# Kernel optimization log

Hardware: AMD Instinct MI355X
Metric: run time of the kernel (lower is better)

The kernel has to match this reference:

```python
import jax, jax.numpy as jnp
import numpy as np

TOPK = 2  # config.topk_exp


def setup_inputs() -> dict:
    key = jax.random.key(0)
    ks = jax.random.split(key, 4)
    B, S, D, F, E = 4, 1024, 768, 3072, 8
    scale_in = 1.0 / np.sqrt(D)
    scale_hid = 1.0 / np.sqrt(F)
    return {
        "x": jax.random.normal(ks[0], (B, S, D), dtype=jnp.float32),
        "router_w": jax.random.normal(ks[1], (E, D), dtype=jnp.float32) * scale_in,
        "w_fc": jax.random.normal(ks[2], (E, D, F), dtype=jnp.float32) * scale_in,
        "b_fc": jnp.zeros((E, F), dtype=jnp.float32),
        "w_proj": jax.random.normal(ks[3], (E, F, D), dtype=jnp.float32) * scale_hid,
        "b_proj": jnp.zeros((E, D), dtype=jnp.float32),
    }


def _moe_forward(x, router_w, w_fc, b_fc, w_proj, b_proj):
    B, S, D = x.shape
    E = router_w.shape[0]
    xt = x.reshape(-1, D)  # [T, D] tokens
    # per-token router: Linear(D, E, bias=False)
    gate_logits = xt @ router_w.T  # [T, E]
    # topk_exp > 1: raw logits -> topk -> softmax over the k selected logits
    weights, selected = jax.lax.top_k(gate_logits, TOPK)  # [T, k]
    weights = jax.nn.softmax(weights.astype(jnp.float32), axis=1).astype(x.dtype)
    # combine weights per expert: w[t, e] = sum_k weights[t,k] * (selected[t,k]==e)
    onehot = jax.nn.one_hot(selected, E, dtype=x.dtype)  # [T, k, E]
    comb = jnp.einsum('tk,tke->te', weights, onehot)  # [T, E]
    # expert MLP (GPT-2 style: fc -> gelu -> proj), evaluated densely then combined
    h = jax.nn.gelu(jnp.einsum('td,edf->etf', xt, w_fc) + b_fc[:, None, :], approximate=False)
    y = jnp.einsum('etf,efd->etd', h, w_proj) + b_proj[:, None, :]  # [E, T, D]
    out = jnp.einsum('te,etd->td', comb, y)  # weighted scatter-combine
    return out.reshape(B, S, D)


def reference(x, router_w, w_fc, b_fc, w_proj, b_proj):
    return _moe_forward(x, router_w, w_fc, b_fc, w_proj, b_proj)
```

## Files before the change

### kernel.cpp

```cpp
#include <hip/hip_runtime.h>
#include <hip/hip_bf16.h>

#define TT 4096
#define DD 768
#define FF 3072
#define EE 8
#define NSLOT 8192
#define NSLOT_PAD 8320

#define WVM0  0x0F70

typedef __attribute__((ext_vector_type(8))) short bf16x8;
typedef __attribute__((ext_vector_type(4))) float f32x4;
typedef const __attribute__((address_space(1))) void* gas1_t;
typedef __attribute__((address_space(3))) void* las3_t;

__global__ __launch_bounds__(256) void router2_kernel(const float* __restrict__ x,
    const float* __restrict__ rw, int* __restrict__ tokE, float* __restrict__ tokW,
    int* __restrict__ blkCnt) {
  __shared__ float rws[EE * 832];
  __shared__ int cnt_s[EE];
  int tid = threadIdx.x;
  if (tid < EE) cnt_s[tid] = 0;
#pragma unroll
  for (int k = 0; k < 6; ++k) {
    int c = tid + k * 256;
    int e = c / 192, rem = c % 192;
    int s = rem / 12, i = rem % 12;
    float4 v = *(const float4*)&rw[e * DD + s * 48 + i * 4];
    *(float4*)&rws[e * 832 + s * 52 + i * 4] = v;
  }
  __syncthreads();
  int lane = tid & 63;
  int sl = lane & 15;
  int t = blockIdx.x * 16 + (tid >> 6) * 4 + (lane >> 4);
  const float4* xp = (const float4*)(x + (size_t)t * DD + sl * 48);
  float acc[EE];
#pragma unroll
  for (int e = 0; e < EE; ++e) acc[e] = 0.f;
#pragma unroll
  for (int i = 0; i < 12; ++i) {
    float4 xv = xp[i];
#pragma unroll
    for (int e = 0; e < EE; ++e) {
      float4 rv = *(const float4*)&rws[e * 832 + sl * 52 + i * 4];
      acc[e] = fmaf(xv.x, rv.x, fmaf(xv.y, rv.y, fmaf(xv.z, rv.z, fmaf(xv.w, rv.w, acc[e]))));
    }
  }
#pragma unroll
  for (int off = 8; off > 0; off >>= 1) {
#pragma unroll
    for (int e = 0; e < EE; ++e) acc[e] += __shfl_xor(acc[e], off);
  }
  if (sl == 0) {
    float v0 = -1e30f; int e0 = 0;
#pragma unroll
    for (int e = 0; e < EE; ++e) { if (acc[e] > v0) { v0 = acc[e]; e0 = e; } }
    float v1 = -1e30f; int e1 = 0;
#pragma unroll
    for (int e = 0; e < EE; ++e) { if (e != e0 && acc[e] > v1) { v1 = acc[e]; e1 = e; } }
    float w1 = 1.f / (1.f + __expf(v0 - v1));
    float w0 = 1.f - w1;
    tokE[2 * t] = e0; tokE[2 * t + 1] = e1;
    tokW[2 * t] = w0; tokW[2 * t + 1] = w1;
    atomicAdd(&cnt_s[e0], 1);
    atomicAdd(&cnt_s[e1], 1);
  }
  __syncthreads();
  if (tid < EE) blkCnt[blockIdx.x * EE + tid] = cnt_s[tid];
}

__global__ __launch_bounds__(256) void offsets2_kernel(const int* __restrict__ blkCnt,
    int* __restrict__ offs, int* __restrict__ blkBase,
    int* __restrict__ tile1, int* __restrict__ tile2, int* __restrict__ meta) {
  __shared__ int wsum[4][EE];
  int tid = threadIdx.x;
  int lane = tid & 63, w = tid >> 6;
  int c[EE], s[EE];
#pragma unroll
  for (int e = 0; e < EE; ++e) { c[e] = blkCnt[tid * EE + e]; s[e] = c[e]; }
#pragma unroll
  for (int off = 1; off < 64; off <<= 1) {
#pragma unroll
    for (int e = 0; e < EE; ++e) {
      int v = __shfl_up(s[e], off);
      if (lane >= off) s[e] += v;
    }
  }
  if (lane == 63) {
#pragma unroll
    for (int e = 0; e < EE; ++e) wsum[w][e] = s[e];
  }
  __syncthreads();
#pragma unroll
  for (int e = 0; e < EE; ++e) {
    int pre = 0;
    for (int w2 = 0; w2 < w; ++w2) pre += wsum[w2][e];
    s[e] += pre;
  }
  int tot[EE];
#pragma unroll
  for (int e = 0; e < EE; ++e) tot[e] = wsum[0][e] + wsum[1][e] + wsum[2][e] + wsum[3][e];
  int offl[EE + 1];
  offl[0] = 0;
#pragma unroll
  for (int e = 0; e < EE; ++e) offl[e + 1] = offl[e] + tot[e];
#pragma unroll
  for (int e = 0; e < EE; ++e) blkBase[tid * EE + e] = offl[e] + s[e] - c[e];
  if (tid == 0) {
    for (int e = 0; e <= EE; ++e) offs[e] = offl[e];
    int n1 = 0, n2 = 0;
    for (int e = 0; e < EE; ++e) { n1 += (tot[e] + 127) / 128; n2 += (tot[e] + 63) / 64; }
    meta[0] = n1; meta[1] = n2;
  }
  if (tid < EE) {
    int p1 = 0, p2 = 0;
    for (int e = 0; e < tid; ++e) { p1 += (tot[e] + 127) / 128; p2 += (tot[e] + 63) / 64; }
    for (int m = 0; m < tot[tid]; m += 128) tile1[p1++] = (tid << 20) | m;
    for (int m = 0; m < tot[tid]; m += 64)  tile2[p2++] = (tid << 20) | m;
  }
}

__global__ __launch_bounds__(256) void scatter_gather2_kernel(const float* __restrict__ x,
    const int* __restrict__ tokE, const float* __restrict__ tokW,
    const int* __restrict__ blkBase, int* __restrict__ slotIdx, float* __restrict__ slotW,
    int* __restrict__ slotTok, __hip_bfloat16* __restrict__ Xg) {
  __shared__ int base_s[EE], lcur[EE];
  __shared__ int sl_s[16][2];
  int tid = threadIdx.x;
  int b = blockIdx.x;
  if (tid < EE) { base_s[tid] = blkBase[b * EE + tid]; lcur[tid] = 0; }
  __syncthreads();
  if (tid < 16) {
    int t = b * 16 + tid;
    int e0 = tokE[2 * t], e1 = tokE[2 * t + 1];
    int s0 = base_s[e0] + atomicAdd(&lcur[e0], 1);
    int s1 = base_s[e1] + atomicAdd(&lcur[e1], 1);
    slotIdx[2 * t] = s0; slotIdx[2 * t + 1] = s1;
    slotW[s0] = tokW[2 * t]; slotW[s1] = tokW[2 * t + 1];
    slotTok[s0] = t; slotTok[s1] = t;
    sl_s[tid][0] = s0; sl_s[tid][1] = s1;
  }
  __syncthreads();
  int k = tid >> 4, p = tid & 15;
  int t = b * 16 + k;
  int s0 = sl_s[k][0], s1 = sl_s[k][1];
  const float4* src = (const float4*)(x + (size_t)t * DD);
  ushort4* d0 = (ushort4*)(Xg + (size_t)s0 * DD);
  ushort4* d1 = (ushort4*)(Xg + (size_t)s1 * DD);
#pragma unroll
  for (int i = 0; i < 12; ++i) {
    int idx = i * 16 + p;
    float4 v = src[idx];
    union { ushort4 u; __hip_bfloat16 h[4]; } cv;
    cv.h[0] = __float2bfloat16(v.x);
    cv.h[1] = __float2bfloat16(v.y);
    cv.h[2] = __float2bfloat16(v.z);
    cv.h[3] = __float2bfloat16(v.w);
    d0[idx] = cv.u;
    d1[idx] = cv.u;
  }
}

__global__ void transpose_convert_kernel(const float* __restrict__ w_fc, __hip_bfloat16* __restrict__ wfcT,
                                         const float* __restrict__ w_proj, __hip_bfloat16* __restrict__ wprojT) {
  __shared__ float tile[64][65];
  int bx = blockIdx.x;
  const float* S; __hip_bfloat16* D; int K, N, n0, k0;
  if (bx < 576) { S = w_fc;   D = wfcT;   K = DD; N = FF; n0 = (bx % 48) * 64; k0 = (bx / 48) * 64; }
  else { bx -= 576; S = w_proj; D = wprojT; K = FF; N = DD; n0 = (bx % 12) * 64; k0 = (bx / 12) * 64; }
  S += (size_t)blockIdx.z * K * N;
  D += (size_t)blockIdx.z * K * N;
  int tid = threadIdx.x;
#pragma unroll
  for (int i = 0; i < 4; ++i) {
    int slot = i * 256 + tid;
    int r = slot >> 4, c4 = slot & 15;
    float4 v = *(const float4*)&S[(size_t)(k0 + r) * N + n0 + c4 * 4];
    tile[r][c4 * 4 + 0] = v.x; tile[r][c4 * 4 + 1] = v.y;
    tile[r][c4 * 4 + 2] = v.z; tile[r][c4 * 4 + 3] = v.w;
  }
  __syncthreads();
#pragma unroll
  for (int i = 0; i < 4; ++i) {
    int slot = i * 256 + tid;
    int n = slot >> 4, kc = slot & 15;
    union { ushort4 u; __hip_bfloat16 h[4]; } cv;
    cv.h[0] = __float2bfloat16(tile[kc * 4 + 0][n]);
    cv.h[1] = __float2bfloat16(tile[kc * 4 + 1][n]);
    cv.h[2] = __float2bfloat16(tile[kc * 4 + 2][n]);
    cv.h[3] = __float2bfloat16(tile[kc * 4 + 3][n]);
    *(ushort4*)&D[(size_t)(n0 + n) * K + k0 + kc * 4] = cv.u;
  }
}

__device__ __forceinline__ float gelu_f(float v) {
  float z = v * 0.70710678118654752f;
  float az = fabsf(z);
  float t = 1.0f / (1.0f + 0.3275911f * az);
  float poly = t * (0.254829592f + t * (-0.284496736f + t * (1.421413741f +
               t * (-1.453152027f + t * 1.061405429f))));
  float erf_abs = 1.0f - poly * __expf(-az * az);
  float erf = copysignf(erf_abs, z);
  return 0.5f * v * (1.0f + erf);
}

#define G_ISSUE(NXT) \
  _Pragma("unroll") for (int i = 0; i < 4; ++i) { \
    __builtin_amdgcn_global_load_lds((gas1_t)gA[i], (las3_t)(&As[NXT][0] + fsd[i]), 16, 0, 0); \
    __builtin_amdgcn_global_load_lds((gas1_t)gB[i], (las3_t)(&Bs[NXT][0] + fsd[i]), 16, 0, 0); \
    gA[i] += 64; gB[i] += 64; }

#define G_COMP(CUR) \
  { const short* cA = &As[CUR][0]; const short* cB = &Bs[CUR][0]; \
    _Pragma("unroll") for (int s = 0; s < 2; ++s) { \
      bf16x8 af[4], bfr[4]; \
      _Pragma("unroll") for (int mi = 0; mi < 4; ++mi) af[mi] = *(const bf16x8*)(cA + aoff[mi][s]); \
      _Pragma("unroll") for (int ni = 0; ni < 4; ++ni) bfr[ni] = *(const bf16x8*)(cB + boff[ni][s]); \
      _Pragma("unroll") for (int mi = 0; mi < 4; ++mi) \
        _Pragma("unroll") for (int ni = 0; ni < 4; ++ni) \
          acc[mi][ni] = __builtin_amdgcn_mfma_f32_16x16x32_bf16(af[mi], bfr[ni], acc[mi][ni], 0, 0, 0); } }

#define S_MAIN(CUR, NXT) \
  __builtin_amdgcn_s_waitcnt(WVM0); \
  __builtin_amdgcn_s_barrier(); \
  G_ISSUE(NXT) \
  G_COMP(CUR)

#define S_LAST(CUR) \
  __builtin_amdgcn_s_waitcnt(WVM0); \
  __builtin_amdgcn_s_barrier(); \
  G_COMP(CUR)

#define GEMM_SETUP(STRIDE) \
  int tid = threadIdx.x; \
  int lane = tid & 63, wid = tid >> 6; \
  int l15 = lane & 15, q = lane >> 4; \
  int wm = wid & 1, wn = wid >> 1; \
  int fsd[4]; \
  const short* gA[4]; \
  const short* gB[4]; \
  _Pragma("unroll") for (int i = 0; i < 4; ++i) { \
    int fs = tid + i * 256; \
    int m = fs >> 3, c = (fs & 7) ^ (m & 7); \
    fsd[i] = fs * 8; \
    gA[i] = A + (size_t)m * STRIDE + c * 8; \
    gB[i] = B + (size_t)m * STRIDE + c * 8; \
  } \
  int aoff[4][2], boff[4][2]; \
  _Pragma("unroll") for (int mi = 0; mi < 4; ++mi) { \
    int r = wm * 64 + mi * 16 + l15; \
    _Pragma("unroll") for (int s = 0; s < 2; ++s) \
      aoff[mi][s] = r * 64 + ((((s << 2) | q) ^ (r & 7)) * 8); \
  } \
  _Pragma("unroll") for (int ni = 0; ni < 4; ++ni) { \
    int r = wn * 64 + ni * 16 + l15; \
    _Pragma("unroll") for (int s = 0; s < 2; ++s) \
      boff[ni][s] = r * 64 + ((((s << 2) | q) ^ (r & 7)) * 8); \
  } \
  f32x4 acc[4][4] = {};

__global__ __launch_bounds__(256) void gemm1_kernel(const __hip_bfloat16* __restrict__ Xg,
    const __hip_bfloat16* __restrict__ wfcT, const float* __restrict__ b_fc,
    __hip_bfloat16* __restrict__ H, const int* __restrict__ offs,
    const int* __restrict__ tile1, const int* __restrict__ meta) {
  __shared__ __align__(16) short As[2][128 * 64];
  __shared__ __align__(16) short Bs[2][128 * 64];
  int wg = blockIdx.x + 24 * blockIdx.y;
  int wl = (wg & 7) * 216 + (wg >> 3);
  int bx = wl % 24;
  int by = wl / 24;
  if (by >= meta[0]) return;
  int tv = tile1[by];
  int e = tv >> 20;
  int m_base = tv & 0xFFFFF;
  int off_e = offs[e];
  int n_e = offs[e + 1] - off_e;
  int n0 = bx * 128;
  const short* A = (const short*)Xg + (size_t)(off_e + m_base) * DD;
  const short* B = (const short*)wfcT + (size_t)e * FF * DD + (size_t)n0 * DD;
  GEMM_SETUP(DD)
  G_ISSUE(0)
  for (int g = 0; g < 5; ++g) {
    S_MAIN(0, 1)
    S_MAIN(1, 0)
  }
  S_MAIN(0, 1)
  S_LAST(1)
  float bias[4];
#pragma unroll
  for (int ni = 0; ni < 4; ++ni) bias[ni] = b_fc[e * FF + n0 + wn * 64 + ni * 16 + l15];
  __hip_bfloat16* Hp = H + (size_t)(off_e + m_base) * FF + n0;
#pragma unroll
  for (int mi = 0; mi < 4; ++mi) {
#pragma unroll
    for (int r = 0; r < 4; ++r) {
      int ml = wm * 64 + mi * 16 + q * 4 + r;
      if (m_base + ml < n_e) {
#pragma unroll
        for (int ni = 0; ni < 4; ++ni) {
          int nl = wn * 64 + ni * 16 + l15;
          float v = acc[mi][ni][r] + bias[ni];
          Hp[(size_t)ml * FF + nl] = __float2bfloat16(gelu_f(v));
        }
      }
    }
  }
}

__global__ __launch_bounds__(256) void gemm2_kernel(const __hip_bfloat16* __restrict__ H,
    const __hip_bfloat16* __restrict__ wprojT, const float* __restrict__ b_proj,
    const float* __restrict__ slotW, const int* __restrict__ slotTok,
    float* __restrict__ out, const int* __restrict__ offs,
    const int* __restrict__ tile1, const int* __restrict__ meta) {
  __shared__ __align__(16) short As[2][128 * 64];
  __shared__ __align__(16) short Bs[2][128 * 64];
  int wg = blockIdx.x + 6 * blockIdx.y;
  int wl = (wg & 7) * 54 + (wg >> 3);
  int bx = wl % 6;
  int by = wl / 6;
  if (by >= meta[0]) return;
  int tv = tile1[by];
  int e = tv >> 20;
  int m_base = tv & 0xFFFFF;
  int off_e = offs[e];
  int n_e = offs[e + 1] - off_e;
  int n0 = bx * 128;
  const short* A = (const short*)H + (size_t)(off_e + m_base) * FF;
  const short* B = (const short*)wprojT + (size_t)e * DD * FF + (size_t)n0 * FF;
  GEMM_SETUP(FF)
  G_ISSUE(0)
  for (int g = 0; g < 23; ++g) {
    S_MAIN(0, 1)
    S_MAIN(1, 0)
  }
  S_MAIN(0, 1)
  S_LAST(1)
  float bias[4];
#pragma unroll
  for (int ni = 0; ni < 4; ++ni)
    bias[ni] = b_proj[e * DD + n0 + wn * 64 + ni * 16 + l15];
#pragma unroll
  for (int mi = 0; mi < 4; ++mi) {
#pragma unroll
    for (int r = 0; r < 4; ++r) {
      int ml = wm * 64 + mi * 16 + q * 4 + r;
      if (m_base + ml < n_e) {
        int slot = off_e + m_base + ml;
        float w = slotW[slot];
        int tok = slotTok[slot];
        float* op = out + (size_t)tok * DD + n0 + wn * 64;
#pragma unroll
        for (int ni = 0; ni < 4; ++ni)
          atomicAdd(&op[ni * 16 + l15], w * (acc[mi][ni][r] + bias[ni]));
      }
    }
  }
}

extern "C" void kernel_launch(void* const* d_in, const int* in_sizes, int n_in,
                              void* d_out, int out_size, void* d_ws, size_t ws_size,
                              hipStream_t stream) {
  const float* x        = (const float*)d_in[0];
  const float* router_w = (const float*)d_in[1];
  const float* w_fc     = (const float*)d_in[2];
  const float* b_fc     = (const float*)d_in[3];
  const float* w_proj   = (const float*)d_in[4];
  const float* b_proj   = (const float*)d_in[5];
  float* out = (float*)d_out;

  char* p = (char*)d_ws;
  auto alloc = [&](size_t bytes) {
    char* r = p;
    p += (bytes + 255) & ~(size_t)255;
    return r;
  };
  __hip_bfloat16* wfcT   = (__hip_bfloat16*)alloc((size_t)EE * FF * DD * 2);
  __hip_bfloat16* wprojT = (__hip_bfloat16*)alloc((size_t)EE * DD * FF * 2);
  __hip_bfloat16* Xg     = (__hip_bfloat16*)alloc((size_t)NSLOT_PAD * DD * 2);
  __hip_bfloat16* H      = (__hip_bfloat16*)alloc((size_t)NSLOT_PAD * FF * 2);
  int*   tokE    = (int*)alloc(TT * 2 * 4);
  float* tokW    = (float*)alloc(TT * 2 * 4);
  int*   slotIdx = (int*)alloc(TT * 2 * 4);
  float* slotW   = (float*)alloc(NSLOT_PAD * 4);
  int*   slotTok = (int*)alloc(NSLOT_PAD * 4);
  int*   blkCnt  = (int*)alloc(256 * EE * 4);
  int*   blkBase = (int*)alloc(256 * EE * 4);
  int*   tile1   = (int*)alloc(128 * 4);
  int*   tile2   = (int*)alloc(256 * 4);
  int*   offs    = (int*)alloc(64);
  int*   meta    = (int*)alloc(64);

  hipMemsetAsync(out, 0, (size_t)out_size * 4, stream);
  router2_kernel<<<256, 256, 0, stream>>>(x, router_w, tokE, tokW, blkCnt);
  offsets2_kernel<<<1, 256, 0, stream>>>(blkCnt, offs, blkBase, tile1, tile2, meta);
  scatter_gather2_kernel<<<256, 256, 0, stream>>>(x, tokE, tokW, blkBase, slotIdx, slotW, slotTok, Xg);
  transpose_convert_kernel<<<dim3(1152, 1, EE), 256, 0, stream>>>(w_fc, wfcT, w_proj, wprojT);
  gemm1_kernel<<<dim3(24, 72), 256, 0, stream>>>(Xg, wfcT, b_fc, H, offs, tile1, meta);
  gemm2_kernel<<<dim3(6, 72), 256, 0, stream>>>(H, wprojT, b_proj, slotW, slotTok, out, offs, tile1, meta);
}
```

Baseline: 353.6 us.

## Enlarge gemm1 tiles to 256x256 with 512 threads and fast reciprocal GELU

The first expert GEMM moves from 128x128 tiles with 256 threads to 256x256 tiles with 512 threads (8 waves, each computing 128x64). Tile scheduling switches to 256-row tiles, and the slot padding grows so the larger tiles stay in bounds. The goal is more data reuse per LDS load and fewer workgroups. The LDS fragment offsets now derive the second k-slice with an XOR, which removes an offset array. The GELU reciprocal uses the hardware v_rcp_f32 instead of a full divide. The larger tile uses 128 KB of LDS and more accumulator registers, so occupancy and tail padding waste are risks.

After: 340.8 us. 3.6% less time.

```diff
diff --git a/kernel.cpp b/kernel.cpp
--- a/kernel.cpp
+++ b/kernel.cpp
@@ -6,7 +6,7 @@
 #define FF 3072
 #define EE 8
 #define NSLOT 8192
-#define NSLOT_PAD 8320
+#define NSLOT_PAD 8448
 
 #define WVM0  0x0F70
 
@@ -110,14 +110,14 @@
   if (tid == 0) {
     for (int e = 0; e <= EE; ++e) offs[e] = offl[e];
     int n1 = 0, n2 = 0;
-    for (int e = 0; e < EE; ++e) { n1 += (tot[e] + 127) / 128; n2 += (tot[e] + 63) / 64; }
+    for (int e = 0; e < EE; ++e) { n1 += (tot[e] + 127) / 128; n2 += (tot[e] + 255) / 256; }
     meta[0] = n1; meta[1] = n2;
   }
   if (tid < EE) {
     int p1 = 0, p2 = 0;
-    for (int e = 0; e < tid; ++e) { p1 += (tot[e] + 127) / 128; p2 += (tot[e] + 63) / 64; }
+    for (int e = 0; e < tid; ++e) { p1 += (tot[e] + 127) / 128; p2 += (tot[e] + 255) / 256; }
     for (int m = 0; m < tot[tid]; m += 128) tile1[p1++] = (tid << 20) | m;
-    for (int m = 0; m < tot[tid]; m += 64)  tile2[p2++] = (tid << 20) | m;
+    for (int m = 0; m < tot[tid]; m += 256) tile2[p2++] = (tid << 20) | m;
   }
 }
 
@@ -194,10 +194,14 @@
   }
 }
 
+__device__ __forceinline__ float rcp_fast(float x) {
+  float r; asm("v_rcp_f32 %0, %1" : "=v"(r) : "v"(x)); return r;
+}
+
 __device__ __forceinline__ float gelu_f(float v) {
   float z = v * 0.70710678118654752f;
   float az = fabsf(z);
-  float t = 1.0f / (1.0f + 0.3275911f * az);
+  float t = rcp_fast(1.0f + 0.3275911f * az);
   float poly = t * (0.254829592f + t * (-0.284496736f + t * (1.421413741f +
                t * (-1.453152027f + t * 1.061405429f))));
   float erf_abs = 1.0f - poly * __expf(-az * az);
@@ -215,8 +219,8 @@
   { const short* cA = &As[CUR][0]; const short* cB = &Bs[CUR][0]; \
     _Pragma("unroll") for (int s = 0; s < 2; ++s) { \
       bf16x8 af[4], bfr[4]; \
-      _Pragma("unroll") for (int mi = 0; mi < 4; ++mi) af[mi] = *(const bf16x8*)(cA + aoff[mi][s]); \
-      _Pragma("unroll") for (int ni = 0; ni < 4; ++ni) bfr[ni] = *(const bf16x8*)(cB + boff[ni][s]); \
+      _Pragma("unroll") for (int mi = 0; mi < 4; ++mi) af[mi] = *(const bf16x8*)(cA + (aoff[mi] ^ (s * 32))); \
+      _Pragma("unroll") for (int ni = 0; ni < 4; ++ni) bfr[ni] = *(const bf16x8*)(cB + (boff[ni] ^ (s * 32))); \
       _Pragma("unroll") for (int mi = 0; mi < 4; ++mi) \
         _Pragma("unroll") for (int ni = 0; ni < 4; ++ni) \
           acc[mi][ni] = __builtin_amdgcn_mfma_f32_16x16x32_bf16(af[mi], bfr[ni], acc[mi][ni], 0, 0, 0); } }
@@ -231,82 +235,6 @@
   __builtin_amdgcn_s_waitcnt(WVM0); \
   __builtin_amdgcn_s_barrier(); \
   G_COMP(CUR)
-
-#define GEMM_SETUP(STRIDE) \
-  int tid = threadIdx.x; \
-  int lane = tid & 63, wid = tid >> 6; \
-  int l15 = lane & 15, q = lane >> 4; \
-  int wm = wid & 1, wn = wid >> 1; \
-  int fsd[4]; \
-  const short* gA[4]; \
-  const short* gB[4]; \
-  _Pragma("unroll") for (int i = 0; i < 4; ++i) { \
-    int fs = tid + i * 256; \
-    int m = fs >> 3, c = (fs & 7) ^ (m & 7); \
-    fsd[i] = fs * 8; \
-    gA[i] = A + (size_t)m * STRIDE + c * 8; \
-    gB[i] = B + (size_t)m * STRIDE + c * 8; \
-  } \
-  int aoff[4][2], boff[4][2]; \
-  _Pragma("unroll") for (int mi = 0; mi < 4; ++mi) { \
-    int r = wm * 64 + mi * 16 + l15; \
-    _Pragma("unroll") for (int s = 0; s < 2; ++s) \
-      aoff[mi][s] = r * 64 + ((((s << 2) | q) ^ (r & 7)) * 8); \
-  } \
-  _Pragma("unroll") for (int ni = 0; ni < 4; ++ni) { \
-    int r = wn * 64 + ni * 16 + l15; \
-    _Pragma("unroll") for (int s = 0; s < 2; ++s) \
-      boff[ni][s] = r * 64 + ((((s << 2) | q) ^ (r & 7)) * 8); \
-  } \
-  f32x4 acc[4][4] = {};
-
-__global__ __launch_bounds__(256) void gemm1_kernel(const __hip_bfloat16* __restrict__ Xg,
-    const __hip_bfloat16* __restrict__ wfcT, const float* __restrict__ b_fc,
-    __hip_bfloat16* __restrict__ H, const int* __restrict__ offs,
-    const int* __restrict__ tile1, const int* __restrict__ meta) {
-  __shared__ __align__(16) short As[2][128 * 64];
-  __shared__ __align__(16) short Bs[2][128 * 64];
-  int wg = blockIdx.x + 24 * blockIdx.y;
-  int wl = (wg & 7) * 216 + (wg >> 3);
-  int bx = wl % 24;
-  int by = wl / 24;
-  if (by >= meta[0]) return;
-  int tv = tile1[by];
-  int e = tv >> 20;
-  int m_base = tv & 0xFFFFF;
-  int off_e = offs[e];
-  int n_e = offs[e + 1] - off_e;
-  int n0 = bx * 128;
-  const short* A = (const short*)Xg + (size_t)(off_e + m_base) * DD;
-  const short* B = (const short*)wfcT + (size_t)e * FF * DD + (size_t)n0 * DD;
-  GEMM_SETUP(DD)
-  G_ISSUE(0)
-  for (int g = 0; g < 5; ++g) {
-    S_MAIN(0, 1)
-    S_MAIN(1, 0)
-  }
-  S_MAIN(0, 1)
-  S_LAST(1)
-  float bias[4];
-#pragma unroll
-  for (int ni = 0; ni < 4; ++ni) bias[ni] = b_fc[e * FF + n0 + wn * 64 + ni * 16 + l15];
-  __hip_bfloat16* Hp = H + (size_t)(off_e + m_base) * FF + n0;
-#pragma unroll
-  for (int mi = 0; mi < 4; ++mi) {
-#pragma unroll
-    for (int r = 0; r < 4; ++r) {
-      int ml = wm * 64 + mi * 16 + q * 4 + r;
-      if (m_base + ml < n_e) {
-#pragma unroll
-        for (int ni = 0; ni < 4; ++ni) {
-          int nl = wn * 64 + ni * 16 + l15;
-          float v = acc[mi][ni][r] + bias[ni];
-          Hp[(size_t)ml * FF + nl] = __float2bfloat16(gelu_f(v));
-        }
-      }
-    }
-  }
-}
 
 __global__ __launch_bounds__(256) void gemm2_kernel(const __hip_bfloat16* __restrict__ H,
     const __hip_bfloat16* __restrict__ wprojT, const float* __restrict__ b_proj,
@@ -328,7 +256,33 @@
   int n0 = bx * 128;
   const short* A = (const short*)H + (size_t)(off_e + m_base) * FF;
   const short* B = (const short*)wprojT + (size_t)e * DD * FF + (size_t)n0 * FF;
-  GEMM_SETUP(FF)
+  int tid = threadIdx.x;
+  int lane = tid & 63, wid = tid >> 6;
+  int l15 = lane & 15, q = lane >> 4;
+  int wm = wid & 1, wn = wid >> 1;
+  int fsd[4];
+  const short* gA[4];
+  const short* gB[4];
+#pragma unroll
+  for (int i = 0; i < 4; ++i) {
+    int fs = tid + i * 256;
+    int m = fs >> 3, c = (fs & 7) ^ (m & 7);
+    fsd[i] = fs * 8;
+    gA[i] = A + (size_t)m * FF + c * 8;
+    gB[i] = B + (size_t)m * FF + c * 8;
+  }
+  int aoff[4], boff[4];
+#pragma unroll
+  for (int mi = 0; mi < 4; ++mi) {
+    int r = wm * 64 + mi * 16 + l15;
+    aoff[mi] = r * 64 + ((q ^ (r & 7)) * 8);
+  }
+#pragma unroll
+  for (int ni = 0; ni < 4; ++ni) {
+    int r = wn * 64 + ni * 16 + l15;
+    boff[ni] = r * 64 + ((q ^ (r & 7)) * 8);
+  }
+  f32x4 acc[4][4] = {};
   G_ISSUE(0)
   for (int g = 0; g < 23; ++g) {
     S_MAIN(0, 1)
@@ -353,6 +307,107 @@
 #pragma unroll
         for (int ni = 0; ni < 4; ++ni)
           atomicAdd(&op[ni * 16 + l15], w * (acc[mi][ni][r] + bias[ni]));
+      }
+    }
+  }
+}
+
+#define G1_ISSUE(NXT) \
+  _Pragma("unroll") for (int i = 0; i < 4; ++i) { \
+    __builtin_amdgcn_global_load_lds((gas1_t)gA[i], (las3_t)(&As[NXT][0] + fsd[i]), 16, 0, 0); \
+    __builtin_amdgcn_global_load_lds((gas1_t)gB[i], (las3_t)(&Bs[NXT][0] + fsd[i]), 16, 0, 0); \
+    gA[i] += 64; gB[i] += 64; }
+
+#define G1_COMP(CUR) \
+  { const short* cA = &As[CUR][0]; const short* cB = &Bs[CUR][0]; \
+    _Pragma("unroll") for (int s = 0; s < 2; ++s) { \
+      bf16x8 af[8], bfr[4]; \
+      _Pragma("unroll") for (int mi = 0; mi < 8; ++mi) af[mi] = *(const bf16x8*)(cA + (aoff[mi] ^ (s * 32))); \
+      _Pragma("unroll") for (int ni = 0; ni < 4; ++ni) bfr[ni] = *(const bf16x8*)(cB + (boff[ni] ^ (s * 32))); \
+      _Pragma("unroll") for (int mi = 0; mi < 8; ++mi) \
+        _Pragma("unroll") for (int ni = 0; ni < 4; ++ni) \
+          acc[mi][ni] = __builtin_amdgcn_mfma_f32_16x16x32_bf16(af[mi], bfr[ni], acc[mi][ni], 0, 0, 0); } }
+
+#define S1_MAIN(CUR, NXT) \
+  __builtin_amdgcn_s_waitcnt(WVM0); \
+  __builtin_amdgcn_s_barrier(); \
+  G1_ISSUE(NXT) \
+  G1_COMP(CUR)
+
+#define S1_LAST(CUR) \
+  __builtin_amdgcn_s_waitcnt(WVM0); \
+  __builtin_amdgcn_s_barrier(); \
+  G1_COMP(CUR)
+
+__global__ __launch_bounds__(512, 2) void gemm1_kernel(const __hip_bfloat16* __restrict__ Xg,
+    const __hip_bfloat16* __restrict__ wfcT, const float* __restrict__ b_fc,
+    __hip_bfloat16* __restrict__ H, const int* __restrict__ offs,
+    const int* __restrict__ tile2, const int* __restrict__ meta) {
+  __shared__ __align__(16) short As[2][256 * 64];
+  __shared__ __align__(16) short Bs[2][256 * 64];
+  int wg = blockIdx.x + 12 * blockIdx.y;
+  int wl = (wg & 7) * 60 + (wg >> 3);
+  int bx = wl % 12;
+  int by = wl / 12;
+  if (by >= meta[1]) return;
+  int tv = tile2[by];
+  int e = tv >> 20;
+  int m_base = tv & 0xFFFFF;
+  int off_e = offs[e];
+  int n_e = offs[e + 1] - off_e;
+  int n0 = bx * 256;
+  const short* A = (const short*)Xg + (size_t)(off_e + m_base) * DD;
+  const short* B = (const short*)wfcT + (size_t)e * FF * DD + (size_t)n0 * DD;
+  int tid = threadIdx.x;
+  int lane = tid & 63, wid = tid >> 6;
+  int l15 = lane & 15, q = lane >> 4;
+  int wm = wid & 1, wn = wid >> 1;
+  int fsd[4];
+  const short* gA[4];
+  const short* gB[4];
+#pragma unroll
+  for (int i = 0; i < 4; ++i) {
+    int fs = tid + i * 512;
+    int m = fs >> 3, c = (fs & 7) ^ (m & 7);
+    fsd[i] = fs * 8;
+    gA[i] = A + (size_t)m * DD + c * 8;
+    gB[i] = B + (size_t)m * DD + c * 8;
+  }
+  int aoff[8], boff[4];
+#pragma unroll
+  for (int mi = 0; mi < 8; ++mi) {
+    int r = wm * 128 + mi * 16 + l15;
+    aoff[mi] = r * 64 + ((q ^ (r & 7)) * 8);
+  }
+#pragma unroll
+  for (int ni = 0; ni < 4; ++ni) {
+    int r = wn * 64 + ni * 16 + l15;
+    boff[ni] = r * 64 + ((q ^ (r & 7)) * 8);
+  }
+  f32x4 acc[8][4] = {};
+  G1_ISSUE(0)
+  for (int g = 0; g < 5; ++g) {
+    S1_MAIN(0, 1)
+    S1_MAIN(1, 0)
+  }
+  S1_MAIN(0, 1)
+  S1_LAST(1)
+  float bias[4];
+#pragma unroll
+  for (int ni = 0; ni < 4; ++ni) bias[ni] = b_fc[e * FF + n0 + wn * 64 + ni * 16 + l15];
+  __hip_bfloat16* Hp = H + (size_t)(off_e + m_base) * FF + n0;
+#pragma unroll
+  for (int mi = 0; mi < 8; ++mi) {
+#pragma unroll
+    for (int r = 0; r < 4; ++r) {
+      int ml = wm * 128 + mi * 16 + q * 4 + r;
+      if (m_base + ml < n_e) {
+#pragma unroll
+        for (int ni = 0; ni < 4; ++ni) {
+          int nl = wn * 64 + ni * 16 + l15;
+          float v = acc[mi][ni][r] + bias[ni];
+          Hp[(size_t)ml * FF + nl] = __float2bfloat16(gelu_f(v));
+        }
       }
     }
   }
@@ -396,6 +451,6 @@
   offsets2_kernel<<<1, 256, 0, stream>>>(blkCnt, offs, blkBase, tile1, tile2, meta);
   scatter_gather2_kernel<<<256, 256, 0, stream>>>(x, tokE, tokW, blkBase, slotIdx, slotW, slotTok, Xg);
   transpose_convert_kernel<<<dim3(1152, 1, EE), 256, 0, stream>>>(w_fc, wfcT, w_proj, wprojT);
-  gemm1_kernel<<<dim3(24, 72), 256, 0, stream>>>(Xg, wfcT, b_fc, H, offs, tile1, meta);
+  gemm1_kernel<<<dim3(12, 40), 512, 0, stream>>>(Xg, wfcT, b_fc, H, offs, tile2, meta);
   gemm2_kernel<<<dim3(6, 72), 256, 0, stream>>>(H, wprojT, b_proj, slotW, slotTok, out, offs, tile1, meta);
 }
```
